# Kernel tuning notes

Measured on AMD Instinct MI355X. Metric: run time of the kernel, lower is better.

## Reference

```python
import jax, jax.numpy as jnp
import numpy as np

L = 8          # n_layer
D = 512        # hidden_size
DIN = 1024     # d_inner = 2*D (Mamba expand=2)
DS = 16        # d_state
DTR = 32       # dt_rank = ceil(D/16)
K = 4          # d_conv
NACT = 3       # n_action_to_predict
ADIM = 4
LOSS_COEF = 1.0

def silu(x):
    return x * jax.nn.sigmoid(x)

def rms(x, w, eps=1e-5):
    return x * jax.lax.rsqrt(jnp.mean(x * x, axis=-1, keepdims=True) + eps) * w

def tokenize(images, states, actions, patch_w, patch_b, state_w, state_b, act_w, act_b):
    # images [b,l,3,224,224] -> 14x14 patches of 3*16*16=768 -> mean-pooled image token
    b, l = images.shape[:2]
    p = images.reshape(b, l, 3, 14, 16, 14, 16).transpose(0, 1, 3, 5, 2, 4, 6).reshape(b, l, 196, 768)
    img = jnp.mean(p @ patch_w.T + patch_b, axis=2)            # [b,l,D] token_type 1
    st = states[:, :, 0] @ state_w.T + state_b                 # [b,l,D] token_type 2
    ac = actions[:, :, :NACT - 1] @ act_w.T + act_b            # [b,l,NACT-1,D] token_type 3
    toks = jnp.concatenate([img[:, :, None], st[:, :, None], ac], axis=2)  # [b,l,1+NACT,D]
    return toks.reshape(b, l * (1 + NACT), D)

def mamba_mixer(x, in_w, cw, cb, xpw, dtw, dtb, alog, dp, ow):
    # x: [b,S,D]
    b, S, _ = x.shape
    xz = x @ in_w.T                                   # [b,S,2*DIN]
    xi, z = xz[..., :DIN], xz[..., DIN:]
    # causal depthwise conv, kernel K
    xp = jnp.pad(xi, ((0, 0), (K - 1, 0), (0, 0)))
    xc = cb + sum(cw[:, k] * xp[:, k:k + S, :] for k in range(K))
    xc = silu(xc)
    proj = xc @ xpw.T                                  # [b,S,DTR+2*DS]
    dtr, Bm, Cm = proj[..., :DTR], proj[..., DTR:DTR + DS], proj[..., DTR + DS:]
    dt = jax.nn.softplus(dtr @ dtw.T + dtb)            # [b,S,DIN]
    A = -jnp.exp(alog)                                 # [DIN,DS]
    dA = jnp.exp(dt[..., None] * A)                    # [b,S,DIN,DS]
    dBx = dt[..., None] * Bm[:, :, None, :] * xc[..., None]
    def step(h, inp):
        a_t, bx_t = inp
        h = a_t * h + bx_t
        return h, h
    _, hs = jax.lax.scan(step, jnp.zeros((b, DIN, DS), x.dtype),
                         (dA.swapaxes(0, 1), dBx.swapaxes(0, 1)))  # hs [S,b,DIN,DS]
    y = jnp.einsum('sbdn,bsn->bsd', hs, Cm) + dp * xc
    return (y * silu(z)) @ ow.T

def _forward(images, seq_length, states, actions, action_labels,
             patch_w, patch_b, state_w, state_b, act_w, act_b,
             norm1_w, in_proj_w, conv_w, conv_b, x_proj_w, dt_w, dt_b,
             A_log, Dp, out_proj_w, norm2_w, fc1_w, fc2_w, norm_f_w,
             head_w, head_b):
    b, l = images.shape[:2]
    hidden = tokenize(images, states, actions, patch_w, patch_b, state_w, state_b, act_w, act_b)
    residual = jnp.zeros_like(hidden)
    for i in range(L):
        residual = hidden + residual
        hidden = mamba_mixer(rms(residual, norm1_w[i]), in_proj_w[i], conv_w[i], conv_b[i],
                             x_proj_w[i], dt_w[i], dt_b[i], A_log[i], Dp[i], out_proj_w[i])
        residual = hidden + residual
        g = rms(residual, norm2_w[i]) @ fc1_w[i].T       # GatedMLP fc1 -> [.., 2*DIN]
        hidden = (g[..., :DIN] * silu(g[..., DIN:])) @ fc2_w[i].T
    residual = hidden + residual
    hidden = rms(residual, norm_f_w)
    # static action-token positions: per-frame tokens [img, state, act, act] -> indices 1..3
    hs = hidden.reshape(b, l, 1 + NACT, D)[:, :, 1:, :]
    action_preds = hs @ head_w.T + head_b                # [b,l,NACT,ADIM]
    mask = (jnp.arange(l)[None, :] < seq_length[:, None]).astype(jnp.float32)
    la = jnp.mean(jnp.abs(action_preds - action_labels), axis=(2, 3))
    la = (la * mask).sum(axis=1) / jnp.clip(mask.sum(axis=1), 1.0)
    loss = jnp.mean(la) * LOSS_COEF
    return loss, action_preds

def setup_inputs() -> dict:
    key = jax.random.key(0)
    ks = iter(jax.random.split(key, 40))
    nrm = lambda shape, s=0.02: s * jax.random.normal(next(ks), shape, dtype=jnp.float32)
    inp = {
        'images': jax.random.normal(next(ks), (2, 64, 3, 224, 224), jnp.float32),
        'seq_length': jax.random.randint(next(ks), (2,), 1, 65),
        'states': jax.random.normal(next(ks), (2, 64, NACT, 7), jnp.float32),
        'actions': jax.random.normal(next(ks), (2, 64, NACT, ADIM), jnp.float32),
        'action_labels': jax.random.normal(next(ks), (2, 64, NACT, ADIM), jnp.float32),
        'patch_w': nrm((D, 768)), 'patch_b': jnp.zeros((D,), jnp.float32),
        'state_w': nrm((D, 7)), 'state_b': jnp.zeros((D,), jnp.float32),
        'act_w': nrm((D, ADIM)), 'act_b': jnp.zeros((D,), jnp.float32),
        'norm1_w': jnp.ones((L, D), jnp.float32),
        'in_proj_w': nrm((L, 2 * DIN, D)),
        'conv_w': nrm((L, DIN, K), 0.1), 'conv_b': jnp.zeros((L, DIN), jnp.float32),
        'x_proj_w': nrm((L, DTR + 2 * DS, DIN)),
        'dt_w': nrm((L, DIN, DTR)), 'dt_b': jnp.full((L, DIN), -4.6, jnp.float32),
        'A_log': jnp.log(jnp.broadcast_to(jnp.arange(1, DS + 1, dtype=jnp.float32), (L, DIN, DS))).copy(),
        'Dp': jnp.ones((L, DIN), jnp.float32),
        'out_proj_w': nrm((L, D, DIN)),
        'norm2_w': jnp.ones((L, D), jnp.float32),
        'fc1_w': nrm((L, 2 * DIN, D)), 'fc2_w': nrm((L, D, DIN)),
        'norm_f_w': jnp.ones((D,), jnp.float32),
        'head_w': nrm((ADIM, D)), 'head_b': jnp.zeros((ADIM,), jnp.float32),
    }
    return inp

def reference(images, seq_length, states, actions, action_labels,
              patch_w, patch_b, state_w, state_b, act_w, act_b,
              norm1_w, in_proj_w, conv_w, conv_b, x_proj_w, dt_w, dt_b,
              A_log, Dp, out_proj_w, norm2_w, fc1_w, fc2_w, norm_f_w,
              head_w, head_b):
    return _forward(images, seq_length, states, actions, action_labels,
                    patch_w, patch_b, state_w, state_b, act_w, act_b,
                    norm1_w, in_proj_w, conv_w, conv_b, x_proj_w, dt_w, dt_b,
                    A_log, Dp, out_proj_w, norm2_w, fc1_w, fc2_w, norm_f_w,
                    head_w, head_b)
```

## Files before the change

### kernel.cpp

```cpp
#include <hip/hip_runtime.h>


#define NTOK 512
#define SEQ  256
#define CS   32
#define NC   8

typedef __attribute__((ext_vector_type(8))) short bf16x8;
typedef __attribute__((ext_vector_type(16))) float f32x16;

__device__ __forceinline__ float silu_f(float x) { return x / (1.0f + expf(-x)); }
__device__ __forceinline__ float softplus_f(float x) {
  return (x > 20.0f) ? x : log1pf(expf(x));
}

__device__ __forceinline__ void split_pack(float4 v, uint2* hi, uint2* lo) {
  uint ux = __float_as_uint(v.x), uy = __float_as_uint(v.y);
  uint uz = __float_as_uint(v.z), uw = __float_as_uint(v.w);
  hi->x = (ux >> 16) | (uy & 0xffff0000u);
  hi->y = (uz >> 16) | (uw & 0xffff0000u);
  float lx = v.x - __uint_as_float(ux & 0xffff0000u);
  float ly = v.y - __uint_as_float(uy & 0xffff0000u);
  float lz = v.z - __uint_as_float(uz & 0xffff0000u);
  float lw = v.w - __uint_as_float(uw & 0xffff0000u);
  lo->x = (__float_as_uint(lx) >> 16) | (__float_as_uint(ly) & 0xffff0000u);
  lo->y = (__float_as_uint(lz) >> 16) | (__float_as_uint(lw) & 0xffff0000u);
}

__global__ __launch_bounds__(256) void gemm_bs_k(const float* __restrict__ A,
                                                 const float* __restrict__ B,
                                                 float* __restrict__ C,
                                                 int M, int N, int K, int Kc) {
  __shared__ alignas(16) ushort sAh[2][2][512];
  __shared__ alignas(16) ushort sAl[2][2][512];
  __shared__ alignas(16) ushort sBh[2][2][512];
  __shared__ alignas(16) ushort sBl[2][2][512];
  int t = threadIdx.x;
  int bn = blockIdx.x, bm = blockIdx.y, z = blockIdx.z;
  const float* Ab = A + (size_t)bm * 64 * K + (size_t)z * Kc;
  const float* Bb = B + (size_t)bn * 64 * K + (size_t)z * Kc;
  float* Cb = C + (size_t)z * M * N;
  int r = t >> 2, kc = (t & 3) << 2;
  int st = r >> 5, m = r & 31;
  int off = ((kc >> 3) << 8) + (m << 3) + (kc & 7);
  int w = t >> 6, lane = t & 63;
  int wr = w >> 1, wc = w & 1;

  f32x16 acc;
#pragma unroll
  for (int i = 0; i < 16; ++i) acc[i] = 0.f;

  int nk = Kc >> 4;
  float4 a4 = *(const float4*)&Ab[(size_t)r * K + kc];
  float4 b4 = *(const float4*)&Bb[(size_t)r * K + kc];
  {
    uint2 hi, lo;
    split_pack(a4, &hi, &lo);
    *(uint2*)&sAh[0][st][off] = hi; *(uint2*)&sAl[0][st][off] = lo;
    split_pack(b4, &hi, &lo);
    *(uint2*)&sBh[0][st][off] = hi; *(uint2*)&sBl[0][st][off] = lo;
  }
  __syncthreads();
  for (int ks = 0; ks < nk; ++ks) {
    int buf = ks & 1;
    if (ks + 1 < nk) {
      a4 = *(const float4*)&Ab[(size_t)r * K + (ks + 1) * 16 + kc];
      b4 = *(const float4*)&Bb[(size_t)r * K + (ks + 1) * 16 + kc];
    }
    bf16x8 ah = *(bf16x8*)&sAh[buf][wr][lane << 3];
    bf16x8 al = *(bf16x8*)&sAl[buf][wr][lane << 3];
    bf16x8 bh = *(bf16x8*)&sBh[buf][wc][lane << 3];
    bf16x8 bl = *(bf16x8*)&sBl[buf][wc][lane << 3];
    acc = __builtin_amdgcn_mfma_f32_32x32x16_bf16(ah, bh, acc, 0, 0, 0);
    acc = __builtin_amdgcn_mfma_f32_32x32x16_bf16(al, bh, acc, 0, 0, 0);
    acc = __builtin_amdgcn_mfma_f32_32x32x16_bf16(ah, bl, acc, 0, 0, 0);
    if (ks + 1 < nk) {
      uint2 hi, lo;
      split_pack(a4, &hi, &lo);
      *(uint2*)&sAh[buf ^ 1][st][off] = hi; *(uint2*)&sAl[buf ^ 1][st][off] = lo;
      split_pack(b4, &hi, &lo);
      *(uint2*)&sBh[buf ^ 1][st][off] = hi; *(uint2*)&sBl[buf ^ 1][st][off] = lo;
    }
    __syncthreads();
  }
  int col = lane & 31, rq = lane >> 5;
  float* Cw = Cb + (size_t)(bm * 64 + wr * 32) * N + bn * 64 + wc * 32 + col;
#pragma unroll
  for (int rg = 0; rg < 16; ++rg) {
    int row = (rg & 3) + ((rg >> 2) << 3) + (rq << 2);
    Cw[(size_t)row * N] = acc[rg];
  }
}

__global__ __launch_bounds__(256) void gemm_glu_k(const float* __restrict__ G,
                                                  const float* __restrict__ B,
                                                  float* __restrict__ C,
                                                  int M, int N, int K, int Kc) {
  __shared__ alignas(16) ushort sAh[2][2][512];
  __shared__ alignas(16) ushort sAl[2][2][512];
  __shared__ alignas(16) ushort sBh[2][2][512];
  __shared__ alignas(16) ushort sBl[2][2][512];
  int t = threadIdx.x;
  int bn = blockIdx.x, bm = blockIdx.y, z = blockIdx.z;
  const float* Gb = G + (size_t)bm * 64 * 2048 + (size_t)z * Kc;
  const float* Bb = B + (size_t)bn * 64 * K + (size_t)z * Kc;
  float* Cb = C + (size_t)z * M * N;
  int r = t >> 2, kc = (t & 3) << 2;
  int st = r >> 5, m = r & 31;
  int off = ((kc >> 3) << 8) + (m << 3) + (kc & 7);
  int w = t >> 6, lane = t & 63;
  int wr = w >> 1, wc = w & 1;

  f32x16 acc;
#pragma unroll
  for (int i = 0; i < 16; ++i) acc[i] = 0.f;

  int nk = Kc >> 4;
  const float* gr = Gb + (size_t)r * 2048 + kc;
  float4 ga = *(const float4*)&gr[0];
  float4 gz = *(const float4*)&gr[1024];
  float4 b4 = *(const float4*)&Bb[(size_t)r * K + kc];
  {
    float4 a4 = {ga.x * silu_f(gz.x), ga.y * silu_f(gz.y),
                 ga.z * silu_f(gz.z), ga.w * silu_f(gz.w)};
    uint2 hi, lo;
    split_pack(a4, &hi, &lo);
    *(uint2*)&sAh[0][st][off] = hi; *(uint2*)&sAl[0][st][off] = lo;
    split_pack(b4, &hi, &lo);
    *(uint2*)&sBh[0][st][off] = hi; *(uint2*)&sBl[0][st][off] = lo;
  }
  __syncthreads();
  for (int ks = 0; ks < nk; ++ks) {
    int buf = ks & 1;
    if (ks + 1 < nk) {
      ga = *(const float4*)&gr[(ks + 1) * 16];
      gz = *(const float4*)&gr[1024 + (ks + 1) * 16];
      b4 = *(const float4*)&Bb[(size_t)r * K + (ks + 1) * 16 + kc];
    }
    bf16x8 ah = *(bf16x8*)&sAh[buf][wr][lane << 3];
    bf16x8 al = *(bf16x8*)&sAl[buf][wr][lane << 3];
    bf16x8 bh = *(bf16x8*)&sBh[buf][wc][lane << 3];
    bf16x8 bl = *(bf16x8*)&sBl[buf][wc][lane << 3];
    acc = __builtin_amdgcn_mfma_f32_32x32x16_bf16(ah, bh, acc, 0, 0, 0);
    acc = __builtin_amdgcn_mfma_f32_32x32x16_bf16(al, bh, acc, 0, 0, 0);
    acc = __builtin_amdgcn_mfma_f32_32x32x16_bf16(ah, bl, acc, 0, 0, 0);
    if (ks + 1 < nk) {
      float4 a4 = {ga.x * silu_f(gz.x), ga.y * silu_f(gz.y),
                   ga.z * silu_f(gz.z), ga.w * silu_f(gz.w)};
      uint2 hi, lo;
      split_pack(a4, &hi, &lo);
      *(uint2*)&sAh[buf ^ 1][st][off] = hi; *(uint2*)&sAl[buf ^ 1][st][off] = lo;
      split_pack(b4, &hi, &lo);
      *(uint2*)&sBh[buf ^ 1][st][off] = hi; *(uint2*)&sBl[buf ^ 1][st][off] = lo;
    }
    __syncthreads();
  }
  int col = lane & 31, rq = lane >> 5;
  float* Cw = Cb + (size_t)(bm * 64 + wr * 32) * N + bn * 64 + wc * 32 + col;
#pragma unroll
  for (int rg = 0; rg < 16; ++rg) {
    int row = (rg & 3) + ((rg >> 2) << 3) + (rq << 2);
    Cw[(size_t)row * N] = acc[rg];
  }
}

__global__ void patch_part_k(const float* __restrict__ img, float* __restrict__ pmp) {
  int blk = blockIdx.x;
  int bl = blk / 14, hb = blk % 14;
  int t = threadIdx.x;
  int c = t >> 6, hi = (t >> 2) & 15, wi4 = t & 3;
  const float* base = img + (size_t)bl * 3 * 50176 + (size_t)c * 50176 +
                      (size_t)(hb * 16 + hi) * 224 + wi4 * 4;
  float4 s = {0.f, 0.f, 0.f, 0.f};
#pragma unroll
  for (int wb = 0; wb < 14; ++wb) {
    float4 v = *(const float4*)&base[wb * 16];
    s.x += v.x; s.y += v.y; s.z += v.z; s.w += v.w;
  }
  ((float4*)(pmp + (size_t)blk * 768))[t] = s;
}

__global__ void patch_red_k(const float* __restrict__ pmp, float* __restrict__ meanp) {
  int bl = blockIdx.x;
  int t = threadIdx.x;
  float4 s = {0.f, 0.f, 0.f, 0.f};
  for (int hb = 0; hb < 14; ++hb) {
    float4 v = ((const float4*)(pmp + (size_t)(bl * 14 + hb) * 768))[t];
    s.x += v.x; s.y += v.y; s.z += v.z; s.w += v.w;
  }
  const float inv = 1.0f / 196.0f;
  float4 o = {s.x * inv, s.y * inv, s.z * inv, s.w * inv};
  ((float4*)(meanp + (size_t)bl * 768))[t] = o;
}

__global__ void tokenize_k(const float* __restrict__ imgp,
                           const float* __restrict__ states,
                           const float* __restrict__ actions,
                           const float* __restrict__ pb,
                           const float* __restrict__ sw, const float* __restrict__ sb,
                           const float* __restrict__ aw, const float* __restrict__ ab,
                           float* __restrict__ hidden, float* __restrict__ residual) {
  int tok = blockIdx.x;
  int t = threadIdx.x;
  int j = tok & 3;
  int bl = tok >> 2;
  int o0 = t * 4;
  float out[4];
  if (j == 0) {
    float4 a = ((const float4*)pb)[t];
    const float* ip = imgp + (size_t)bl * 512;
#pragma unroll
    for (int p = 0; p < 8; ++p) {
      float4 v = ((const float4*)(ip + (size_t)p * 65536))[t];
      a.x += v.x; a.y += v.y; a.z += v.z; a.w += v.w;
    }
    out[0] = a.x; out[1] = a.y; out[2] = a.z; out[3] = a.w;
  } else if (j == 1) {
    const float* sv = states + (size_t)bl * 21;
#pragma unroll
    for (int i = 0; i < 4; ++i) {
      int o = o0 + i;
      float acc = sb[o];
      for (int k = 0; k < 7; ++k) acc += sw[o * 7 + k] * sv[k];
      out[i] = acc;
    }
  } else {
    const float* av = actions + ((size_t)bl * 3 + (j - 2)) * 4;
#pragma unroll
    for (int i = 0; i < 4; ++i) {
      int o = o0 + i;
      float acc = ab[o];
      for (int k = 0; k < 4; ++k) acc += aw[o * 4 + k] * av[k];
      out[i] = acc;
    }
  }
  float4 ov = {out[0], out[1], out[2], out[3]};
  ((float4*)(hidden + (size_t)tok * 512))[t] = ov;
  float4 z4 = {0.f, 0.f, 0.f, 0.f};
  ((float4*)(residual + (size_t)tok * 512))[t] = z4;
}

__global__ void addnorm_k(const float* __restrict__ hid, int parts,
                          float* __restrict__ res,
                          const float* __restrict__ w, float* __restrict__ xn) {
  int tok = blockIdx.x;
  int t = threadIdx.x;
  float4* r4 = (float4*)(res + (size_t)tok * 512);
  float4 r = r4[t];
  const float4* hp = (const float4*)(hid + (size_t)tok * 512);
  for (int p = 0; p < parts; ++p) {
    float4 h = hp[t];
    r.x += h.x; r.y += h.y; r.z += h.z; r.w += h.w;
    hp += 65536;
  }
  r4[t] = r;
  float ss = r.x * r.x + r.y * r.y + r.z * r.z + r.w * r.w;
  for (int off = 32; off; off >>= 1) ss += __shfl_down(ss, off, 64);
  __shared__ float s2[2];
  if ((t & 63) == 0) s2[t >> 6] = ss;
  __syncthreads();
  float tot = s2[0] + s2[1];
  float scale = rsqrtf(tot * (1.0f / 512.0f) + 1e-5f);
  float4 wv = ((const float4*)w)[t];
  float4 o = {r.x * scale * wv.x, r.y * scale * wv.y,
              r.z * scale * wv.z, r.w * scale * wv.w};
  ((float4*)(xn + (size_t)tok * 512))[t] = o;
}

__global__ __launch_bounds__(256) void convproj_k(const float* __restrict__ xz,
                                                  const float* __restrict__ cw,
                                                  const float* __restrict__ cb,
                                                  const float* __restrict__ xpw,
                                                  const float* __restrict__ dtw,
                                                  const float* __restrict__ dtbias,
                                                  float* __restrict__ xc,
                                                  float* __restrict__ proj,
                                                  float* __restrict__ dt) {
  int tok = blockIdx.x;
  int t = threadIdx.x;
  int b = tok >> 8, s = tok & 255;
  __shared__ float xr[1024];
  __shared__ float pp[4][64];
  __shared__ float pr[64];
  int d4 = t * 4;
  float4 cw0 = ((const float4*)cw)[d4];
  float4 cw1 = ((const float4*)cw)[d4 + 1];
  float4 cw2 = ((const float4*)cw)[d4 + 2];
  float4 cw3 = ((const float4*)cw)[d4 + 3];
  float acc0 = cb[d4], acc1 = cb[d4 + 1], acc2 = cb[d4 + 2], acc3 = cb[d4 + 3];
  const float* base = xz + (size_t)b * 256 * 2048 + d4;
  const float wk0[4] = {cw0.x, cw0.y, cw0.z, cw0.w};
  const float wk1[4] = {cw1.x, cw1.y, cw1.z, cw1.w};
  const float wk2[4] = {cw2.x, cw2.y, cw2.z, cw2.w};
  const float wk3[4] = {cw3.x, cw3.y, cw3.z, cw3.w};
#pragma unroll
  for (int k = 0; k < 4; ++k) {
    int row = s + k - 3;
    if (row >= 0) {
      float4 v = *(const float4*)&base[(size_t)row * 2048];
      acc0 += wk0[k] * v.x; acc1 += wk1[k] * v.y;
      acc2 += wk2[k] * v.z; acc3 += wk3[k] * v.w;
    }
  }
  float4 xc4 = {silu_f(acc0), silu_f(acc1), silu_f(acc2), silu_f(acc3)};
  ((float4*)(xc + (size_t)tok * 1024))[t] = xc4;
  *(float4*)&xr[d4] = xc4;
  __syncthreads();
  int n = t & 63, q = t >> 6;
  {
    const float* wrow = xpw + (size_t)n * 1024 + q * 256;
    const float* xq = xr + q * 256;
    float acc = 0.f;
    for (int k = 0; k < 256; k += 4)
      acc += wrow[k] * xq[k] + wrow[k + 1] * xq[k + 1] +
             wrow[k + 2] * xq[k + 2] + wrow[k + 3] * xq[k + 3];
    pp[q][n] = acc;
  }
  __syncthreads();
  if (t < 64) {
    float v = pp[0][t] + pp[1][t] + pp[2][t] + pp[3][t];
    pr[t] = v;
    proj[(size_t)tok * 64 + t] = v;
  }
  __syncthreads();
#pragma unroll
  for (int i = 0; i < 4; ++i) {
    int d = t * 4 + i;
    const float* dw = dtw + (size_t)d * 32;
    float a = dtbias[d];
    for (int k = 0; k < 32; ++k) a += dw[k] * pr[k];
    dt[(size_t)tok * 1024 + d] = softplus_f(a);
  }
}

__global__ __launch_bounds__(128) void scan1_k(const float* __restrict__ dt,
                                               const float* __restrict__ proj,
                                               const float* __restrict__ xc,
                                               const float* __restrict__ alog,
                                               float2* __restrict__ pairs) {
  __shared__ float sDt[CS][8];
  __shared__ float sXc[CS][8];
  __shared__ float sB[CS][16];
  int t = threadIdx.x;
  int g = blockIdx.x, c = blockIdx.y;
  int b = g >> 7;
  int d0 = (g & 127) << 3;
  int dl = t >> 4, n = t & 15;
  int d = d0 + dl;
  int s0 = c * CS;
  float A = -expf(alog[d * 16 + n]);
  const float* dtb = dt + ((size_t)b * SEQ + s0) * 1024 + d0;
  const float* xcb = xc + ((size_t)b * SEQ + s0) * 1024 + d0;
  const float* pbp = proj + ((size_t)b * SEQ + s0) * 64 + 32;
  if (t < 64) {
    int li = t >> 1, lc4 = (t & 1) * 4;
    *(float4*)&sDt[li][lc4] = *(const float4*)&dtb[(size_t)li * 1024 + lc4];
    *(float4*)&sXc[li][lc4] = *(const float4*)&xcb[(size_t)li * 1024 + lc4];
  }
  {
    int r = t >> 2, c4 = (t & 3) * 4;
    *(float4*)&sB[r][c4] = *(const float4*)&pbp[(size_t)r * 64 + c4];
  }
  __syncthreads();
  float Ap = 1.f, Bacc = 0.f;
#pragma unroll
  for (int i = 0; i < CS; ++i) {
    float dtv = sDt[i][dl];
    float dA = __expf(dtv * A);
    Bacc = dA * Bacc + dtv * sB[i][n] * sXc[i][dl];
    Ap *= dA;
  }
  pairs[(((size_t)c * 2 + b) * 1024 + d) * 16 + n] = make_float2(Ap, Bacc);
}

__global__ __launch_bounds__(128) void scan2_k(const float* __restrict__ dt,
                                               const float* __restrict__ proj,
                                               const float* __restrict__ xc,
                                               const float* __restrict__ xz,
                                               const float* __restrict__ alog,
                                               const float* __restrict__ Dp,
                                               const float2* __restrict__ pairs,
                                               float* __restrict__ yz) {
  __shared__ float sDt[CS][8];
  __shared__ float sXc[CS][8];
  __shared__ float sZ[CS][8];
  __shared__ float sBC[CS][32];
  __shared__ float sY[CS][8];
  int t = threadIdx.x;
  int g = blockIdx.x, c = blockIdx.y;
  int b = g >> 7;
  int d0 = (g & 127) << 3;
  int dl = t >> 4, n = t & 15;
  int d = d0 + dl;
  int s0 = c * CS;
  float A = -expf(alog[d * 16 + n]);
  float dp = Dp[d];
  const float* dtb = dt + ((size_t)b * SEQ + s0) * 1024 + d0;
  const float* xcb = xc + ((size_t)b * SEQ + s0) * 1024 + d0;
  const float* zb  = xz + ((size_t)b * SEQ + s0) * 2048 + 1024 + d0;
  const float* pbp = proj + ((size_t)b * SEQ + s0) * 64 + 32;
  float* yb = yz + ((size_t)b * SEQ + s0) * 1024 + d0;
  float h = 0.f;
  for (int cc = 0; cc < c; ++cc) {
    float2 p = pairs[(((size_t)cc * 2 + b) * 1024 + d) * 16 + n];
    h = p.x * h + p.y;
  }
  bool lowh = t < 64;
  int u = lowh ? t : t - 64;
  int li = u >> 1, lc4 = (u & 1) * 4;
  if (lowh) {
    *(float4*)&sDt[li][lc4] = *(const float4*)&dtb[(size_t)li * 1024 + lc4];
    *(float4*)&sXc[li][lc4] = *(const float4*)&xcb[(size_t)li * 1024 + lc4];
  } else {
    *(float4*)&sZ[li][lc4] = *(const float4*)&zb[(size_t)li * 2048 + lc4];
  }
  {
    int v0i = t >> 3, v0c = (t & 7) * 4;
    int v1i = (t + 128) >> 3, v1c = ((t + 128) & 7) * 4;
    *(float4*)&sBC[v0i][v0c] = *(const float4*)&pbp[(size_t)v0i * 64 + v0c];
    *(float4*)&sBC[v1i][v1c] = *(const float4*)&pbp[(size_t)v1i * 64 + v1c];
  }
  __syncthreads();
#pragma unroll
  for (int i = 0; i < CS; ++i) {
    float dtv = sDt[i][dl];
    float xcv = sXc[i][dl];
    float dA = __expf(dtv * A);
    h = dA * h + dtv * sBC[i][n] * xcv;
    float yc = h * sBC[i][16 + n];
    yc += __shfl_xor(yc, 1, 64);
    yc += __shfl_xor(yc, 2, 64);
    yc += __shfl_xor(yc, 4, 64);
    yc += __shfl_xor(yc, 8, 64);
    if (n == 0) sY[i][dl] = (yc + dp * xcv) * silu_f(sZ[i][dl]);
  }
  __syncthreads();
  if (lowh)
    *(float4*)&yb[(size_t)li * 1024 + lc4] = *(const float4*)&sY[li][lc4];
}

__global__ void head_k(const float* __restrict__ hf, const float* __restrict__ hw,
                       const float* __restrict__ hb, const float* __restrict__ labels,
                       float* __restrict__ preds, float* __restrict__ labs) {
  int blk = blockIdx.x;
  int j = blk % 3;
  int l = (blk / 3) % 64;
  int b = blk / 192;
  int row = b * 256 + l * 4 + 1 + j;
  int t = threadIdx.x;
  const float* x = hf + (size_t)row * 512;
  float acc[4] = {0.f, 0.f, 0.f, 0.f};
  for (int k = t; k < 512; k += 64) {
    float xv = x[k];
#pragma unroll
    for (int a = 0; a < 4; ++a) acc[a] += xv * hw[a * 512 + k];
  }
  for (int off = 32; off; off >>= 1) {
#pragma unroll
    for (int a = 0; a < 4; ++a) acc[a] += __shfl_down(acc[a], off, 64);
  }
  if (t == 0) {
    const float* lab = labels + (size_t)blk * 4;
    float sd = 0.f;
#pragma unroll
    for (int a = 0; a < 4; ++a) {
      float p = acc[a] + hb[a];
      preds[(size_t)blk * 4 + a] = p;
      sd += fabsf(p - lab[a]);
    }
    labs[blk] = sd;
  }
}

__global__ void loss_k(const float* __restrict__ labs, const int* __restrict__ seqlen,
                       float* __restrict__ out) {
  int t = threadIdx.x;
  int b = t >> 6, l = t & 63;
  float la = (labs[(b * 64 + l) * 3] + labs[(b * 64 + l) * 3 + 1] +
              labs[(b * 64 + l) * 3 + 2]) * (1.0f / 12.0f);
  float m = (l < seqlen[b]) ? 1.f : 0.f;
  float v = la * m;
  for (int off = 32; off; off >>= 1) {
    v += __shfl_down(v, off, 64);
    m += __shfl_down(m, off, 64);
  }
  __shared__ float sb_[2];
  if ((t & 63) == 0) sb_[b] = v / fmaxf(m, 1.0f);
  __syncthreads();
  if (t == 0) out[0] = 0.5f * (sb_[0] + sb_[1]);
}

extern "C" void kernel_launch(void* const* d_in, const int* in_sizes, int n_in,
                              void* d_out, int out_size, void* d_ws, size_t ws_size,
                              hipStream_t stream) {
  const float* images     = (const float*)d_in[0];
  const int*   seq_length = (const int*)d_in[1];
  const float* states     = (const float*)d_in[2];
  const float* actions    = (const float*)d_in[3];
  const float* labels     = (const float*)d_in[4];
  const float* patch_w    = (const float*)d_in[5];
  const float* patch_b    = (const float*)d_in[6];
  const float* state_w    = (const float*)d_in[7];
  const float* state_b    = (const float*)d_in[8];
  const float* act_w      = (const float*)d_in[9];
  const float* act_b      = (const float*)d_in[10];
  const float* norm1_w    = (const float*)d_in[11];
  const float* in_proj_w  = (const float*)d_in[12];
  const float* conv_w     = (const float*)d_in[13];
  const float* conv_b     = (const float*)d_in[14];
  const float* x_proj_w   = (const float*)d_in[15];
  const float* dt_w       = (const float*)d_in[16];
  const float* dt_b       = (const float*)d_in[17];
  const float* A_log      = (const float*)d_in[18];
  const float* Dp         = (const float*)d_in[19];
  const float* out_proj_w = (const float*)d_in[20];
  const float* norm2_w    = (const float*)d_in[21];
  const float* fc1_w      = (const float*)d_in[22];
  const float* fc2_w      = (const float*)d_in[23];
  const float* norm_f_w   = (const float*)d_in[24];
  const float* head_w     = (const float*)d_in[25];
  const float* head_b     = (const float*)d_in[26];

  float* out = (float*)d_out;

  float* ws = (float*)d_ws;
  float* meanp    = ws; ws += 98304;
  float* hidden   = ws; ws += 262144;
  float* residual = ws; ws += 262144;
  float* xn       = ws; ws += 262144;
  float* xz       = ws; ws += 1048576;
  float* xc       = ws; ws += 524288;
  float* proj     = ws; ws += 32768;
  float* dtbuf    = ws; ws += 524288;
  float* yz       = ws; ws += 524288;
  float* labs     = ws; ws += 384;
  float* cpart    = ws; ws += 1048576;
  float* pmp      = ws; ws += 1376256;
  float2* pairs   = (float2*)ws; ws += 524288;

  hipLaunchKernelGGL(patch_part_k, dim3(1792), dim3(192), 0, stream, images, pmp);
  hipLaunchKernelGGL(patch_red_k, dim3(128), dim3(192), 0, stream, pmp, meanp);
  hipLaunchKernelGGL(gemm_bs_k, dim3(8, 2, 8), dim3(256), 0, stream,
                     meanp, patch_w, cpart, 128, 512, 768, 96);
  hipLaunchKernelGGL(tokenize_k, dim3(512), dim3(128), 0, stream, cpart, states, actions,
                     patch_b, state_w, state_b, act_w, act_b, hidden, residual);

  for (int i = 0; i < 8; ++i) {
    const float* n1 = norm1_w + i * 512;
    const float* ipw = in_proj_w + (size_t)i * 2048 * 512;
    const float* cw = conv_w + (size_t)i * 4096;
    const float* cb = conv_b + (size_t)i * 1024;
    const float* xpw = x_proj_w + (size_t)i * 65536;
    const float* dtw = dt_w + (size_t)i * 32768;
    const float* dtbias = dt_b + (size_t)i * 1024;
    const float* al = A_log + (size_t)i * 16384;
    const float* dpp = Dp + (size_t)i * 1024;
    const float* opw = out_proj_w + (size_t)i * 524288;
    const float* n2 = norm2_w + i * 512;
    const float* f1 = fc1_w + (size_t)i * 1048576;
    const float* f2 = fc2_w + (size_t)i * 524288;

    if (i == 0)
      hipLaunchKernelGGL(addnorm_k, dim3(512), dim3(128), 0, stream,
                         hidden, 1, residual, n1, xn);
    else
      hipLaunchKernelGGL(addnorm_k, dim3(512), dim3(128), 0, stream,
                         cpart, 4, residual, n1, xn);
    hipLaunchKernelGGL(gemm_bs_k, dim3(32, 8, 1), dim3(256), 0, stream,
                       xn, ipw, xz, 512, 2048, 512, 512);
    hipLaunchKernelGGL(convproj_k, dim3(512), dim3(256), 0, stream,
                       xz, cw, cb, xpw, dtw, dtbias, xc, proj, dtbuf);
    hipLaunchKernelGGL(scan1_k, dim3(256, 8), dim3(128), 0, stream,
                       dtbuf, proj, xc, al, pairs);
    hipLaunchKernelGGL(scan2_k, dim3(256, 8), dim3(128), 0, stream,
                       dtbuf, proj, xc, xz, al, dpp, pairs, yz);
    hipLaunchKernelGGL(gemm_bs_k, dim3(8, 8, 4), dim3(256), 0, stream,
                       yz, opw, cpart, 512, 512, 1024, 256);
    hipLaunchKernelGGL(addnorm_k, dim3(512), dim3(128), 0, stream,
                       cpart, 4, residual, n2, xn);
    hipLaunchKernelGGL(gemm_bs_k, dim3(32, 8, 1), dim3(256), 0, stream,
                       xn, f1, xz, 512, 2048, 512, 512);
    hipLaunchKernelGGL(gemm_glu_k, dim3(8, 8, 4), dim3(256), 0, stream,
                       xz, f2, cpart, 512, 512, 1024, 256);
  }

  hipLaunchKernelGGL(addnorm_k, dim3(512), dim3(128), 0, stream,
                     cpart, 4, residual, norm_f_w, xn);
  hipLaunchKernelGGL(head_k, dim3(384), dim3(64), 0, stream, xn, head_w, head_b, labels,
                     out + 1, labs);
  hipLaunchKernelGGL(loss_k, dim3(1), dim3(128), 0, stream, labs, seq_length, out);
}
```

Before: 1.175 ms.

## Fuse two-pass chunked scan into one block-local kernel; deepen GEMM k-step

The two-kernel chunked selective scan, which passed chunk carries through a global pairs buffer, becomes a single kernel. Each 512-thread block owns 4 channels over the full sequence, stages dt/xc/z/B/C in shared memory, and combines the 8 chunk carries through shared memory. This removes one launch per layer and the global round-trip of the pairs. The GEMM kernels also process 32 k-elements per pipeline stage instead of 16, halving barriers and loop iterations at the cost of doubled shared memory and registers. The scan grid shrinks from 2048 small blocks to 512 large ones, which may reduce latency hiding.

```diff
diff --git a/kernel.cpp b/kernel.cpp
--- a/kernel.cpp
+++ b/kernel.cpp
@@ -31,10 +31,10 @@
                                                  const float* __restrict__ B,
                                                  float* __restrict__ C,
                                                  int M, int N, int K, int Kc) {
-  __shared__ alignas(16) ushort sAh[2][2][512];
-  __shared__ alignas(16) ushort sAl[2][2][512];
-  __shared__ alignas(16) ushort sBh[2][2][512];
-  __shared__ alignas(16) ushort sBl[2][2][512];
+  __shared__ alignas(16) ushort sAh[2][2][2][512];
+  __shared__ alignas(16) ushort sAl[2][2][2][512];
+  __shared__ alignas(16) ushort sBh[2][2][2][512];
+  __shared__ alignas(16) ushort sBl[2][2][2][512];
   int t = threadIdx.x;
   int bn = blockIdx.x, bm = blockIdx.y, z = blockIdx.z;
   const float* Ab = A + (size_t)bm * 64 * K + (size_t)z * Kc;
@@ -50,36 +50,57 @@
 #pragma unroll
   for (int i = 0; i < 16; ++i) acc[i] = 0.f;
 
-  int nk = Kc >> 4;
-  float4 a4 = *(const float4*)&Ab[(size_t)r * K + kc];
-  float4 b4 = *(const float4*)&Bb[(size_t)r * K + kc];
+  int ns = Kc >> 5;
+  const float* Ar = Ab + (size_t)r * K + kc;
+  const float* Br = Bb + (size_t)r * K + kc;
+  float4 a0 = *(const float4*)&Ar[0];
+  float4 a1 = *(const float4*)&Ar[16];
+  float4 b0 = *(const float4*)&Br[0];
+  float4 b1 = *(const float4*)&Br[16];
   {
     uint2 hi, lo;
-    split_pack(a4, &hi, &lo);
-    *(uint2*)&sAh[0][st][off] = hi; *(uint2*)&sAl[0][st][off] = lo;
-    split_pack(b4, &hi, &lo);
-    *(uint2*)&sBh[0][st][off] = hi; *(uint2*)&sBl[0][st][off] = lo;
-  }
-  __syncthreads();
-  for (int ks = 0; ks < nk; ++ks) {
-    int buf = ks & 1;
-    if (ks + 1 < nk) {
-      a4 = *(const float4*)&Ab[(size_t)r * K + (ks + 1) * 16 + kc];
-      b4 = *(const float4*)&Bb[(size_t)r * K + (ks + 1) * 16 + kc];
-    }
-    bf16x8 ah = *(bf16x8*)&sAh[buf][wr][lane << 3];
-    bf16x8 al = *(bf16x8*)&sAl[buf][wr][lane << 3];
-    bf16x8 bh = *(bf16x8*)&sBh[buf][wc][lane << 3];
-    bf16x8 bl = *(bf16x8*)&sBl[buf][wc][lane << 3];
+    split_pack(a0, &hi, &lo);
+    *(uint2*)&sAh[0][0][st][off] = hi; *(uint2*)&sAl[0][0][st][off] = lo;
+    split_pack(a1, &hi, &lo);
+    *(uint2*)&sAh[0][1][st][off] = hi; *(uint2*)&sAl[0][1][st][off] = lo;
+    split_pack(b0, &hi, &lo);
+    *(uint2*)&sBh[0][0][st][off] = hi; *(uint2*)&sBl[0][0][st][off] = lo;
+    split_pack(b1, &hi, &lo);
+    *(uint2*)&sBh[0][1][st][off] = hi; *(uint2*)&sBl[0][1][st][off] = lo;
+  }
+  __syncthreads();
+  for (int ssi = 0; ssi < ns; ++ssi) {
+    int buf = ssi & 1;
+    if (ssi + 1 < ns) {
+      a0 = *(const float4*)&Ar[(ssi + 1) * 32];
+      a1 = *(const float4*)&Ar[(ssi + 1) * 32 + 16];
+      b0 = *(const float4*)&Br[(ssi + 1) * 32];
+      b1 = *(const float4*)&Br[(ssi + 1) * 32 + 16];
+    }
+    bf16x8 ah = *(bf16x8*)&sAh[buf][0][wr][lane << 3];
+    bf16x8 al = *(bf16x8*)&sAl[buf][0][wr][lane << 3];
+    bf16x8 bh = *(bf16x8*)&sBh[buf][0][wc][lane << 3];
+    bf16x8 bl = *(bf16x8*)&sBl[buf][0][wc][lane << 3];
     acc = __builtin_amdgcn_mfma_f32_32x32x16_bf16(ah, bh, acc, 0, 0, 0);
     acc = __builtin_amdgcn_mfma_f32_32x32x16_bf16(al, bh, acc, 0, 0, 0);
     acc = __builtin_amdgcn_mfma_f32_32x32x16_bf16(ah, bl, acc, 0, 0, 0);
-    if (ks + 1 < nk) {
+    bf16x8 ah1 = *(bf16x8*)&sAh[buf][1][wr][lane << 3];
+    bf16x8 al1 = *(bf16x8*)&sAl[buf][1][wr][lane << 3];
+    bf16x8 bh1 = *(bf16x8*)&sBh[buf][1][wc][lane << 3];
+    bf16x8 bl1 = *(bf16x8*)&sBl[buf][1][wc][lane << 3];
+    acc = __builtin_amdgcn_mfma_f32_32x32x16_bf16(ah1, bh1, acc, 0, 0, 0);
+    acc = __builtin_amdgcn_mfma_f32_32x32x16_bf16(al1, bh1, acc, 0, 0, 0);
+    acc = __builtin_amdgcn_mfma_f32_32x32x16_bf16(ah1, bl1, acc, 0, 0, 0);
+    if (ssi + 1 < ns) {
       uint2 hi, lo;
-      split_pack(a4, &hi, &lo);
-      *(uint2*)&sAh[buf ^ 1][st][off] = hi; *(uint2*)&sAl[buf ^ 1][st][off] = lo;
-      split_pack(b4, &hi, &lo);
-      *(uint2*)&sBh[buf ^ 1][st][off] = hi; *(uint2*)&sBl[buf ^ 1][st][off] = lo;
+      split_pack(a0, &hi, &lo);
+      *(uint2*)&sAh[buf ^ 1][0][st][off] = hi; *(uint2*)&sAl[buf ^ 1][0][st][off] = lo;
+      split_pack(a1, &hi, &lo);
+      *(uint2*)&sAh[buf ^ 1][1][st][off] = hi; *(uint2*)&sAl[buf ^ 1][1][st][off] = lo;
+      split_pack(b0, &hi, &lo);
+      *(uint2*)&sBh[buf ^ 1][0][st][off] = hi; *(uint2*)&sBl[buf ^ 1][0][st][off] = lo;
+      split_pack(b1, &hi, &lo);
+      *(uint2*)&sBh[buf ^ 1][1][st][off] = hi; *(uint2*)&sBl[buf ^ 1][1][st][off] = lo;
     }
     __syncthreads();
   }
@@ -96,10 +117,10 @@
                                                   const float* __restrict__ B,
                                                   float* __restrict__ C,
                                                   int M, int N, int K, int Kc) {
-  __shared__ alignas(16) ushort sAh[2][2][512];
-  __shared__ alignas(16) ushort sAl[2][2][512];
-  __shared__ alignas(16) ushort sBh[2][2][512];
-  __shared__ alignas(16) ushort sBl[2][2][512];
+  __shared__ alignas(16) ushort sAh[2][2][2][512];
+  __shared__ alignas(16) ushort sAl[2][2][2][512];
+  __shared__ alignas(16) ushort sBh[2][2][2][512];
+  __shared__ alignas(16) ushort sBl[2][2][2][512];
   int t = threadIdx.x;
   int bn = blockIdx.x, bm = blockIdx.y, z = blockIdx.z;
   const float* Gb = G + (size_t)bm * 64 * 2048 + (size_t)z * Kc;
@@ -115,43 +136,69 @@
 #pragma unroll
   for (int i = 0; i < 16; ++i) acc[i] = 0.f;
 
-  int nk = Kc >> 4;
+  int ns = Kc >> 5;
   const float* gr = Gb + (size_t)r * 2048 + kc;
-  float4 ga = *(const float4*)&gr[0];
-  float4 gz = *(const float4*)&gr[1024];
-  float4 b4 = *(const float4*)&Bb[(size_t)r * K + kc];
+  const float* Br = Bb + (size_t)r * K + kc;
+  float4 ga0 = *(const float4*)&gr[0];
+  float4 gz0 = *(const float4*)&gr[1024];
+  float4 ga1 = *(const float4*)&gr[16];
+  float4 gz1 = *(const float4*)&gr[1040];
+  float4 b0 = *(const float4*)&Br[0];
+  float4 b1 = *(const float4*)&Br[16];
   {
-    float4 a4 = {ga.x * silu_f(gz.x), ga.y * silu_f(gz.y),
-                 ga.z * silu_f(gz.z), ga.w * silu_f(gz.w)};
+    float4 a0 = {ga0.x * silu_f(gz0.x), ga0.y * silu_f(gz0.y),
+                 ga0.z * silu_f(gz0.z), ga0.w * silu_f(gz0.w)};
+    float4 a1 = {ga1.x * silu_f(gz1.x), ga1.y * silu_f(gz1.y),
+                 ga1.z * silu_f(gz1.z), ga1.w * silu_f(gz1.w)};
     uint2 hi, lo;
-    split_pack(a4, &hi, &lo);
-    *(uint2*)&sAh[0][st][off] = hi; *(uint2*)&sAl[0][st][off] = lo;
-    split_pack(b4, &hi, &lo);
-    *(uint2*)&sBh[0][st][off] = hi; *(uint2*)&sBl[0][st][off] = lo;
-  }
-  __syncthreads();
-  for (int ks = 0; ks < nk; ++ks) {
-    int buf = ks & 1;
-    if (ks + 1 < nk) {
-      ga = *(const float4*)&gr[(ks + 1) * 16];
-      gz = *(const float4*)&gr[1024 + (ks + 1) * 16];
-      b4 = *(const float4*)&Bb[(size_t)r * K + (ks + 1) * 16 + kc];
-    }
-    bf16x8 ah = *(bf16x8*)&sAh[buf][wr][lane << 3];
-    bf16x8 al = *(bf16x8*)&sAl[buf][wr][lane << 3];
-    bf16x8 bh = *(bf16x8*)&sBh[buf][wc][lane << 3];
-    bf16x8 bl = *(bf16x8*)&sBl[buf][wc][lane << 3];
+    split_pack(a0, &hi, &lo);
+    *(uint2*)&sAh[0][0][st][off] = hi; *(uint2*)&sAl[0][0][st][off] = lo;
+    split_pack(a1, &hi, &lo);
+    *(uint2*)&sAh[0][1][st][off] = hi; *(uint2*)&sAl[0][1][st][off] = lo;
+    split_pack(b0, &hi, &lo);
+    *(uint2*)&sBh[0][0][st][off] = hi; *(uint2*)&sBl[0][0][st][off] = lo;
+    split_pack(b1, &hi, &lo);
+    *(uint2*)&sBh[0][1][st][off] = hi; *(uint2*)&sBl[0][1][st][off] = lo;
+  }
+  __syncthreads();
+  for (int ssi = 0; ssi < ns; ++ssi) {
+    int buf = ssi & 1;
+    if (ssi + 1 < ns) {
+      ga0 = *(const float4*)&gr[(ssi + 1) * 32];
+      gz0 = *(const float4*)&gr[1024 + (ssi + 1) * 32];
+      ga1 = *(const float4*)&gr[(ssi + 1) * 32 + 16];
+      gz1 = *(const float4*)&gr[1040 + (ssi + 1) * 32];
+      b0 = *(const float4*)&Br[(ssi + 1) * 32];
+      b1 = *(const float4*)&Br[(ssi + 1) * 32 + 16];
+    }
+    bf16x8 ah = *(bf16x8*)&sAh[buf][0][wr][lane << 3];
+    bf16x8 al = *(bf16x8*)&sAl[buf][0][wr][lane << 3];
+    bf16x8 bh = *(bf16x8*)&sBh[buf][0][wc][lane << 3];
+    bf16x8 bl = *(bf16x8*)&sBl[buf][0][wc][lane << 3];
     acc = __builtin_amdgcn_mfma_f32_32x32x16_bf16(ah, bh, acc, 0, 0, 0);
     acc = __builtin_amdgcn_mfma_f32_32x32x16_bf16(al, bh, acc, 0, 0, 0);
     acc = __builtin_amdgcn_mfma_f32_32x32x16_bf16(ah, bl, acc, 0, 0, 0);
-    if (ks + 1 < nk) {
-      float4 a4 = {ga.x * silu_f(gz.x), ga.y * silu_f(gz.y),
-                   ga.z * silu_f(gz.z), ga.w * silu_f(gz.w)};
+    bf16x8 ah1 = *(bf16x8*)&sAh[buf][1][wr][lane << 3];
+    bf16x8 al1 = *(bf16x8*)&sAl[buf][1][wr][lane << 3];
+    bf16x8 bh1 = *(bf16x8*)&sBh[buf][1][wc][lane << 3];
+    bf16x8 bl1 = *(bf16x8*)&sBl[buf][1][wc][lane << 3];
+    acc = __builtin_amdgcn_mfma_f32_32x32x16_bf16(ah1, bh1, acc, 0, 0, 0);
+    acc = __builtin_amdgcn_mfma_f32_32x32x16_bf16(al1, bh1, acc, 0, 0, 0);
+    acc = __builtin_amdgcn_mfma_f32_32x32x16_bf16(ah1, bl1, acc, 0, 0, 0);
+    if (ssi + 1 < ns) {
+      float4 a0 = {ga0.x * silu_f(gz0.x), ga0.y * silu_f(gz0.y),
+                   ga0.z * silu_f(gz0.z), ga0.w * silu_f(gz0.w)};
+      float4 a1 = {ga1.x * silu_f(gz1.x), ga1.y * silu_f(gz1.y),
+                   ga1.z * silu_f(gz1.z), ga1.w * silu_f(gz1.w)};
       uint2 hi, lo;
-      split_pack(a4, &hi, &lo);
-      *(uint2*)&sAh[buf ^ 1][st][off] = hi; *(uint2*)&sAl[buf ^ 1][st][off] = lo;
-      split_pack(b4, &hi, &lo);
-      *(uint2*)&sBh[buf ^ 1][st][off] = hi; *(uint2*)&sBl[buf ^ 1][st][off] = lo;
+      split_pack(a0, &hi, &lo);
+      *(uint2*)&sAh[buf ^ 1][0][st][off] = hi; *(uint2*)&sAl[buf ^ 1][0][st][off] = lo;
+      split_pack(a1, &hi, &lo);
+      *(uint2*)&sAh[buf ^ 1][1][st][off] = hi; *(uint2*)&sAl[buf ^ 1][1][st][off] = lo;
+      split_pack(b0, &hi, &lo);
+      *(uint2*)&sBh[buf ^ 1][0][st][off] = hi; *(uint2*)&sBl[buf ^ 1][0][st][off] = lo;
+      split_pack(b1, &hi, &lo);
+      *(uint2*)&sBh[buf ^ 1][1][st][off] = hi; *(uint2*)&sBl[buf ^ 1][1][st][off] = lo;
     }
     __syncthreads();
   }
@@ -333,110 +380,83 @@
   }
 }
 
-__global__ __launch_bounds__(128) void scan1_k(const float* __restrict__ dt,
-                                               const float* __restrict__ proj,
-                                               const float* __restrict__ xc,
-                                               const float* __restrict__ alog,
-                                               float2* __restrict__ pairs) {
-  __shared__ float sDt[CS][8];
-  __shared__ float sXc[CS][8];
-  __shared__ float sB[CS][16];
-  int t = threadIdx.x;
-  int g = blockIdx.x, c = blockIdx.y;
-  int b = g >> 7;
-  int d0 = (g & 127) << 3;
-  int dl = t >> 4, n = t & 15;
+__global__ __launch_bounds__(512) void scan_k(const float* __restrict__ dt,
+                                              const float* __restrict__ proj,
+                                              const float* __restrict__ xc,
+                                              const float* __restrict__ xz,
+                                              const float* __restrict__ alog,
+                                              const float* __restrict__ Dp,
+                                              float* __restrict__ yz) {
+  __shared__ float sDt[256][4];
+  __shared__ float sXc[256][4];
+  __shared__ float sZ[256][4];
+  __shared__ float sBC[256][32];
+  __shared__ float2 sP[8][4][16];
+  __shared__ float sY[256][4];
+  int t = threadIdx.x;
+  int g = blockIdx.x;
+  int b = g >> 8;
+  int d0 = (g & 255) << 2;
+  int c = t >> 6, dl = (t >> 4) & 3, n = t & 15;
   int d = d0 + dl;
-  int s0 = c * CS;
-  float A = -expf(alog[d * 16 + n]);
-  const float* dtb = dt + ((size_t)b * SEQ + s0) * 1024 + d0;
-  const float* xcb = xc + ((size_t)b * SEQ + s0) * 1024 + d0;
-  const float* pbp = proj + ((size_t)b * SEQ + s0) * 64 + 32;
-  if (t < 64) {
-    int li = t >> 1, lc4 = (t & 1) * 4;
-    *(float4*)&sDt[li][lc4] = *(const float4*)&dtb[(size_t)li * 1024 + lc4];
-    *(float4*)&sXc[li][lc4] = *(const float4*)&xcb[(size_t)li * 1024 + lc4];
-  }
-  {
-    int r = t >> 2, c4 = (t & 3) * 4;
-    *(float4*)&sB[r][c4] = *(const float4*)&pbp[(size_t)r * 64 + c4];
-  }
-  __syncthreads();
-  float Ap = 1.f, Bacc = 0.f;
-#pragma unroll
-  for (int i = 0; i < CS; ++i) {
-    float dtv = sDt[i][dl];
-    float dA = __expf(dtv * A);
-    Bacc = dA * Bacc + dtv * sB[i][n] * sXc[i][dl];
-    Ap *= dA;
-  }
-  pairs[(((size_t)c * 2 + b) * 1024 + d) * 16 + n] = make_float2(Ap, Bacc);
-}
-
-__global__ __launch_bounds__(128) void scan2_k(const float* __restrict__ dt,
-                                               const float* __restrict__ proj,
-                                               const float* __restrict__ xc,
-                                               const float* __restrict__ xz,
-                                               const float* __restrict__ alog,
-                                               const float* __restrict__ Dp,
-                                               const float2* __restrict__ pairs,
-                                               float* __restrict__ yz) {
-  __shared__ float sDt[CS][8];
-  __shared__ float sXc[CS][8];
-  __shared__ float sZ[CS][8];
-  __shared__ float sBC[CS][32];
-  __shared__ float sY[CS][8];
-  int t = threadIdx.x;
-  int g = blockIdx.x, c = blockIdx.y;
-  int b = g >> 7;
-  int d0 = (g & 127) << 3;
-  int dl = t >> 4, n = t & 15;
-  int d = d0 + dl;
-  int s0 = c * CS;
+  const float* dtb = dt + (size_t)b * 256 * 1024 + d0;
+  const float* xcb = xc + (size_t)b * 256 * 1024 + d0;
+  const float* zb  = xz + (size_t)b * 256 * 2048 + 1024 + d0;
+  const float* pbp = proj + (size_t)b * 256 * 64 + 32;
+  float* yb = yz + (size_t)b * 256 * 1024 + d0;
+
+  if (t < 256) {
+    *(float4*)&sDt[t][0] = *(const float4*)&dtb[(size_t)t * 1024];
+    *(float4*)&sZ[t][0]  = *(const float4*)&zb[(size_t)t * 2048];
+  } else {
+    int u = t - 256;
+    *(float4*)&sXc[u][0] = *(const float4*)&xcb[(size_t)u * 1024];
+  }
+#pragma unroll
+  for (int i = 0; i < 4; ++i) {
+    int idx = i * 512 + t;
+    int s = idx >> 3, c4 = (idx & 7) << 2;
+    *(float4*)&sBC[s][c4] = *(const float4*)&pbp[(size_t)s * 64 + c4];
+  }
   float A = -expf(alog[d * 16 + n]);
   float dp = Dp[d];
-  const float* dtb = dt + ((size_t)b * SEQ + s0) * 1024 + d0;
-  const float* xcb = xc + ((size_t)b * SEQ + s0) * 1024 + d0;
-  const float* zb  = xz + ((size_t)b * SEQ + s0) * 2048 + 1024 + d0;
-  const float* pbp = proj + ((size_t)b * SEQ + s0) * 64 + 32;
-  float* yb = yz + ((size_t)b * SEQ + s0) * 1024 + d0;
+  __syncthreads();
+
+  float Ap = 1.f, Bacc = 0.f;
+#pragma unroll
+  for (int i = 0; i < CS; ++i) {
+    int s = (c << 5) + i;
+    float dtv = sDt[s][dl];
+    float dA = __expf(dtv * A);
+    Bacc = dA * Bacc + dtv * sBC[s][n] * sXc[s][dl];
+    Ap *= dA;
+  }
+  sP[c][dl][n] = make_float2(Ap, Bacc);
+  __syncthreads();
+
   float h = 0.f;
   for (int cc = 0; cc < c; ++cc) {
-    float2 p = pairs[(((size_t)cc * 2 + b) * 1024 + d) * 16 + n];
+    float2 p = sP[cc][dl][n];
     h = p.x * h + p.y;
   }
-  bool lowh = t < 64;
-  int u = lowh ? t : t - 64;
-  int li = u >> 1, lc4 = (u & 1) * 4;
-  if (lowh) {
-    *(float4*)&sDt[li][lc4] = *(const float4*)&dtb[(size_t)li * 1024 + lc4];
-    *(float4*)&sXc[li][lc4] = *(const float4*)&xcb[(size_t)li * 1024 + lc4];
-  } else {
-    *(float4*)&sZ[li][lc4] = *(const float4*)&zb[(size_t)li * 2048 + lc4];
-  }
-  {
-    int v0i = t >> 3, v0c = (t & 7) * 4;
-    int v1i = (t + 128) >> 3, v1c = ((t + 128) & 7) * 4;
-    *(float4*)&sBC[v0i][v0c] = *(const float4*)&pbp[(size_t)v0i * 64 + v0c];
-    *(float4*)&sBC[v1i][v1c] = *(const float4*)&pbp[(size_t)v1i * 64 + v1c];
-  }
-  __syncthreads();
+
 #pragma unroll
   for (int i = 0; i < CS; ++i) {
-    float dtv = sDt[i][dl];
-    float xcv = sXc[i][dl];
+    int s = (c << 5) + i;
+    float dtv = sDt[s][dl];
+    float xcv = sXc[s][dl];
     float dA = __expf(dtv * A);
-    h = dA * h + dtv * sBC[i][n] * xcv;
-    float yc = h * sBC[i][16 + n];
+    h = dA * h + dtv * sBC[s][n] * xcv;
+    float yc = h * sBC[s][16 + n];
     yc += __shfl_xor(yc, 1, 64);
     yc += __shfl_xor(yc, 2, 64);
     yc += __shfl_xor(yc, 4, 64);
     yc += __shfl_xor(yc, 8, 64);
-    if (n == 0) sY[i][dl] = (yc + dp * xcv) * silu_f(sZ[i][dl]);
-  }
-  __syncthreads();
-  if (lowh)
-    *(float4*)&yb[(size_t)li * 1024 + lc4] = *(const float4*)&sY[li][lc4];
+    if (n == 0) sY[s][dl] = (yc + dp * xcv) * silu_f(sZ[s][dl]);
+  }
+  __syncthreads();
+  if (t < 256)
+    *(float4*)&yb[(size_t)t * 1024] = *(const float4*)&sY[t][0];
 }
 
 __global__ void head_k(const float* __restrict__ hf, const float* __restrict__ hw,
@@ -536,7 +556,6 @@
   float* labs     = ws; ws += 384;
   float* cpart    = ws; ws += 1048576;
   float* pmp      = ws; ws += 1376256;
-  float2* pairs   = (float2*)ws; ws += 524288;
 
   hipLaunchKernelGGL(patch_part_k, dim3(1792), dim3(192), 0, stream, images, pmp);
   hipLaunchKernelGGL(patch_red_k, dim3(128), dim3(192), 0, stream, pmp, meanp);
@@ -570,10 +589,8 @@
                        xn, ipw, xz, 512, 2048, 512, 512);
     hipLaunchKernelGGL(convproj_k, dim3(512), dim3(256), 0, stream,
                        xz, cw, cb, xpw, dtw, dtbias, xc, proj, dtbuf);
-    hipLaunchKernelGGL(scan1_k, dim3(256, 8), dim3(128), 0, stream,
-                       dtbuf, proj, xc, al, pairs);
-    hipLaunchKernelGGL(scan2_k, dim3(256, 8), dim3(128), 0, stream,
-                       dtbuf, proj, xc, xz, al, dpp, pairs, yz);
+    hipLaunchKernelGGL(scan_k, dim3(512), dim3(512), 0, stream,
+                       dtbuf, proj, xc, xz, al, dpp, yz);
     hipLaunchKernelGGL(gemm_bs_k, dim3(8, 8, 4), dim3(256), 0, stream,
                        yz, opw, cpart, 512, 512, 1024, 256);
     hipLaunchKernelGGL(addnorm_k, dim3(512), dim3(128), 0, stream,
```

New measurement: 1.117 ms. 4.9% less time.
